# Optimization experiments

Measured on AMD Instinct MI355X. Metric: run time of the kernel, lower is better.

## Reference

```python
import jax, jax.numpy as jnp
import numpy as np

D_MODEL = 512
N_HEADS = 8
MAX_CH = 128
LN_EPS = 1e-5


def setup_inputs() -> dict:
    key = jax.random.key(0)
    ks = jax.random.split(key, 8)
    B, T, C, D = 8, 256, 64, D_MODEL
    x = jax.random.normal(ks[0], (B, T, C, D), dtype=jnp.float32)
    # nn.MultiheadAttention params: packed in_proj [3D, D], out_proj [D, D]
    in_proj_w = jax.random.normal(ks[1], (3 * D, D), dtype=jnp.float32) * 0.02
    in_proj_b = jnp.zeros((3 * D,), dtype=jnp.float32)
    out_proj_w = jax.random.normal(ks[2], (D, D), dtype=jnp.float32) * 0.02
    out_proj_b = jnp.zeros((D,), dtype=jnp.float32)
    ln_g = jnp.ones((D,), dtype=jnp.float32)
    ln_b = jnp.zeros((D,), dtype=jnp.float32)
    rel_pos_bias = jax.random.normal(ks[3], (N_HEADS, MAX_CH, MAX_CH), dtype=jnp.float32) * 0.02
    return {"x": x, "in_proj_w": in_proj_w, "in_proj_b": in_proj_b,
            "out_proj_w": out_proj_w, "out_proj_b": out_proj_b,
            "ln_g": ln_g, "ln_b": ln_b, "rel_pos_bias": rel_pos_bias}


def _layernorm(x, g, b):
    mu = jnp.mean(x, axis=-1, keepdims=True)
    var = jnp.var(x, axis=-1, keepdims=True)
    return (x - mu) * jax.lax.rsqrt(var + LN_EPS) * g + b


def reference(x, in_proj_w, in_proj_b, out_proj_w, out_proj_b, ln_g, ln_b, rel_pos_bias):
    B, T, C, D = x.shape
    H = N_HEADS
    hd = D // H
    N = B * T
    xf = x.reshape(N, C, D)
    # 2D additive attn_mask: mean over heads of rel-pos bias, broadcast over heads/batch
    bias = jnp.mean(rel_pos_bias[:, :C, :C], axis=0)  # [C, C]
    qkv = xf @ in_proj_w.T + in_proj_b  # [N, C, 3D]
    q, k, v = jnp.split(qkv, 3, axis=-1)
    q = q.reshape(N, C, H, hd)
    k = k.reshape(N, C, H, hd)
    v = v.reshape(N, C, H, hd)
    scores = jnp.einsum('nqhd,nkhd->nhqk', q, k) / jnp.sqrt(jnp.float32(hd))
    scores = scores + bias[None, None, :, :]
    attn = jax.nn.softmax(scores, axis=-1)
    ctx = jnp.einsum('nhqk,nkhd->nqhd', attn, v).reshape(N, C, D)
    attn_out = ctx @ out_proj_w.T + out_proj_b
    out = _layernorm(xf + attn_out, ln_g, ln_b)
    return out.reshape(B, T, C, D)
```

## Files before the change

kernel.cpp:

```cpp
#include <hip/hip_runtime.h>
#include <stdint.h>
#include <stddef.h>


typedef __attribute__((ext_vector_type(8))) short short8;
typedef __attribute__((ext_vector_type(4))) float f32x4;

typedef __attribute__((address_space(3))) unsigned int as3_u32;
typedef __attribute__((address_space(1))) unsigned int as1_u32;

#define VMCNT5  asm volatile("s_waitcnt vmcnt(5)" ::: "memory")
#define VMCNT2  asm volatile("s_waitcnt vmcnt(2)" ::: "memory")
#define VMCNT0  asm volatile("s_waitcnt vmcnt(0)" ::: "memory")
#define LGKM0   asm volatile("s_waitcnt lgkmcnt(0)" ::: "memory")
#define BARR()  __builtin_amdgcn_s_barrier()
#define PRIO1   __builtin_amdgcn_s_setprio(1)
#define PRIO0   __builtin_amdgcn_s_setprio(0)

__device__ __forceinline__ unsigned short f2bf(float f) {
  unsigned u = __builtin_bit_cast(unsigned, f);
  u = (u + 0x7FFFu + ((u >> 16) & 1u)) >> 16;
  return (unsigned short)u;
}

__device__ __forceinline__ f32x4 mfma16(short8 a, short8 b, f32x4 c) {
  return __builtin_amdgcn_mfma_f32_16x16x32_bf16(a, b, c, 0, 0, 0);
}

__device__ __forceinline__ short8 rd8s(const char* buf, int row, int unit) {
  return *(const short8*)(buf + row * 128 + ((unit ^ (row & 7)) * 16));
}
__device__ __forceinline__ void wr2s(char* buf, int row, int col, unsigned short v) {
  int slot = (col >> 3) ^ (row & 7);
  *(unsigned short*)(buf + row * 128 + slot * 16 + (col & 7) * 2) = v;
}
__device__ __forceinline__ void wr8s(char* buf, int row, int col, uint2 v) {
  int slot = (col >> 3) ^ (row & 7);
  *(uint2*)(buf + row * 128 + slot * 16 + (col & 7) * 2) = v;
}

__device__ __forceinline__ void stage8w(char* lds, const char* gsrc, int w, int lane) {
  __builtin_amdgcn_global_load_lds((const as1_u32*)(gsrc + w * 1024 + lane * 16),
                                   (as3_u32*)(lds + w * 1024), 16, 0, 0);
}

__device__ __forceinline__ void stage16k(char* ldsbase, const char* gsrc, int w, int lane) {
#pragma unroll
  for (int j = 0; j < 4; ++j) {
    int off = j * 4096 + w * 1024;
    __builtin_amdgcn_global_load_lds((const as1_u32*)(gsrc + off + lane * 16),
                                     (as3_u32*)(ldsbase + off), 16, 0, 0);
  }
}

__global__ void prep_kernel(const float* __restrict__ x,
                            const float* __restrict__ wqkv_f,
                            const float* __restrict__ wo_f,
                            const float* __restrict__ rel,
                            unsigned short* __restrict__ wt,
                            float* __restrict__ bias2d,
                            char* __restrict__ dout) {
  int b = blockIdx.x, tid = threadIdx.x;
  if (b < 8192) {
    int n = b >> 2, p = b & 3;
    char* dstb = dout + (size_t)n * 131072 + 65536;
    const float* srcb = x + (size_t)n * 32768;
#pragma unroll
    for (int t = 0; t < 4; ++t) {
      int flat = t * 256 + tid;
      int c = p * 2 + (flat >> 9);
      int r512 = flat & 511;
      int row = r512 >> 3, u = r512 & 7;
      const float* src = srcb + row * 512 + c * 64 + u * 8;
      float4 a = *(const float4*)src;
      float4 cc = *(const float4*)(src + 4);
      unsigned p0 = (unsigned)f2bf(a.x) | ((unsigned)f2bf(a.y) << 16);
      unsigned p1 = (unsigned)f2bf(a.z) | ((unsigned)f2bf(a.w) << 16);
      unsigned p2 = (unsigned)f2bf(cc.x) | ((unsigned)f2bf(cc.y) << 16);
      unsigned p3 = (unsigned)f2bf(cc.z) | ((unsigned)f2bf(cc.w) << 16);
      *(uint4*)(dstb + c * 8192 + u * 1024 + row * 16) = make_uint4(p0, p1, p2, p3);
    }
  } else if (b < 8288) {
    int cb2 = (b - 8192) * 2;
#pragma unroll
    for (int t = 0; t < 4; ++t) {
      int flat = t * 256 + tid;
      int c = cb2 + (flat >> 9);
      int r512 = flat & 511;
      int row = r512 >> 3, us = r512 & 7;
      int kg = us ^ (row & 7);
      int h = c / 24, j = c % 24;
      int kc = j / 3, rg = j % 3;
      const float* src =
          wqkv_f + (size_t)(rg * 512 + h * 64 + row) * 512 + kc * 64 + kg * 8;
      float4 a = *(const float4*)src;
      float4 cc = *(const float4*)(src + 4);
      unsigned p0 = (unsigned)f2bf(a.x) | ((unsigned)f2bf(a.y) << 16);
      unsigned p1 = (unsigned)f2bf(a.z) | ((unsigned)f2bf(a.w) << 16);
      unsigned p2 = (unsigned)f2bf(cc.x) | ((unsigned)f2bf(cc.y) << 16);
      unsigned p3 = (unsigned)f2bf(cc.z) | ((unsigned)f2bf(cc.w) << 16);
      *(uint4*)(wt + (size_t)c * 4096 + r512 * 8) = make_uint4(p0, p1, p2, p3);
    }
  } else if (b < 8320) {
    int cw = b - 8288;
    unsigned short* dst = wt + 786432 + (size_t)cw * 8192;
#pragma unroll
    for (int t = 0; t < 4; ++t) {
      int u = t * 256 + tid;
      int row = u >> 4, us = u & 15;
      int kg = (us & 8) | ((us ^ row) & 7);
      int kcw = cw >> 3, ng = cw & 7;
      const float* src = wo_f + (size_t)(ng * 64 + row) * 512 + kcw * 128 + kg * 8;
      float4 a = *(const float4*)src;
      float4 cc = *(const float4*)(src + 4);
      unsigned p0 = (unsigned)f2bf(a.x) | ((unsigned)f2bf(a.y) << 16);
      unsigned p1 = (unsigned)f2bf(a.z) | ((unsigned)f2bf(a.w) << 16);
      unsigned p2 = (unsigned)f2bf(cc.x) | ((unsigned)f2bf(cc.y) << 16);
      unsigned p3 = (unsigned)f2bf(cc.z) | ((unsigned)f2bf(cc.w) << 16);
      *(uint4*)(dst + u * 8) = make_uint4(p0, p1, p2, p3);
    }
  } else {
    int idx = (b - 8320) * 256 + tid;
    int m = idx >> 6, nn = idx & 63;
    float s = 0.f;
#pragma unroll
    for (int hh = 0; hh < 8; ++hh) s += rel[hh * 16384 + m * 128 + nn];
    bias2d[idx] = s * 0.125f;
  }
}

__global__ __launch_bounds__(512) void attn_qkv2(
    const char* __restrict__ wq,
    const float* __restrict__ bqkv,
    const float* __restrict__ bias2d,
    char* __restrict__ ctxg) {
  extern __shared__ __attribute__((aligned(16))) char smem[];
  char* RING = smem;
  char* XB   = smem + 32768;
  char* SCb  = smem + 49152;
  float* BQ  = (float*)(smem + 98304);

  const int tid = threadIdx.x;
  const int w = tid >> 6, lane = tid & 63;
  const int l15 = lane & 15, g = lane >> 4;
  const int ws = w >> 2;
  const int wn = w & 3;
  const int n0 = blockIdx.x * 2;

  const char* x0 = ctxg + (size_t)n0 * 131072 + 65536;
  const char* x1 = x0 + 131072;
  char* B0 = SCb + ws * 24576;
  char* B1 = B0 + 8192;
  char* B2 = B0 + 16384;

  const int brow = wn * 16 + l15;
  const int us0 = (g ^ (brow & 7)) * 16;
  const int us1 = ((4 + g) ^ (brow & 7)) * 16;
  const int mrow = wn * 16 + g * 4;
  const int wrow = wn * 16 + l15;

#pragma unroll
  for (int i = 0; i < 3; ++i) BQ[i * 512 + tid] = bqkv[i * 512 + tid];
  float b2d[16];
#pragma unroll
  for (int nt = 0; nt < 4; ++nt)
#pragma unroll
    for (int r = 0; r < 4; ++r)
      b2d[nt * 4 + r] = bias2d[(mrow + r) * 64 + nt * 16 + l15];
  VMCNT0; LGKM0; BARR();

  stage8w(XB, x0, w, lane);
  stage8w(XB + 8192, x1, w, lane);
  stage8w(RING, wq, w, lane);
  stage8w(RING + 8192, wq + 8192, w, lane);
  stage8w(RING + 16384, wq + 16384, w, lane);

  for (int h = 0; h < 8; ++h) {
    f32x4 aq[4] = {}, ak[4] = {}, av[4] = {};
#pragma unroll
    for (int kc = 0; kc < 8; ++kc) {
      const int j = h * 24 + kc * 3;
      const int sQ = (kc * 3) & 3, sK = (kc * 3 + 1) & 3, sV = (kc * 3 + 2) & 3;
      const int tQ = (kc * 3 + 3) & 3, tK = (kc * 3 + 4) & 3, tV = (kc * 3 + 5) & 3;
      { int c = j + 3; if (c > 191) c = 191;
        stage8w(RING + tQ * 8192, wq + (size_t)c * 8192, w, lane); }
      VMCNT2; BARR();
      short8 xa[8];
      { const char* xb = XB + ws * 8192;
#pragma unroll
        for (int mt = 0; mt < 4; ++mt)
#pragma unroll
          for (int ks = 0; ks < 2; ++ks)
            xa[mt * 2 + ks] = *(const short8*)(xb + (ks * 4 + g) * 1024 +
                                               (mt * 16 + l15) * 16);
      }
      {
        const char* wsl = RING + sQ * 8192;
        short8 bf0 = *(const short8*)(wsl + brow * 128 + us0);
        short8 bf1 = *(const short8*)(wsl + brow * 128 + us1);
        PRIO1;
#pragma unroll
        for (int mt = 0; mt < 4; ++mt) {
          aq[mt] = mfma16(xa[mt * 2], bf0, aq[mt]);
          aq[mt] = mfma16(xa[mt * 2 + 1], bf1, aq[mt]);
        }
        PRIO0;
      }
      { int c = j + 4; if (c > 191) c = 191;
        stage8w(RING + tK * 8192, wq + (size_t)c * 8192, w, lane); }
      BARR();
      {
        const char* wsl = RING + sK * 8192;
        short8 bf0 = *(const short8*)(wsl + brow * 128 + us0);
        short8 bf1 = *(const short8*)(wsl + brow * 128 + us1);
        PRIO1;
#pragma unroll
        for (int mt = 0; mt < 4; ++mt) {
          ak[mt] = mfma16(xa[mt * 2], bf0, ak[mt]);
          ak[mt] = mfma16(xa[mt * 2 + 1], bf1, ak[mt]);
        }
        PRIO0;
      }
      { int k2 = (kc + 1) & 7;
        stage8w(XB, x0 + (size_t)k2 * 8192, w, lane);
        stage8w(XB + 8192, x1 + (size_t)k2 * 8192, w, lane); }
      { int c = j + 5; if (c > 191) c = 191;
        stage8w(RING + tV * 8192, wq + (size_t)c * 8192, w, lane); }
      VMCNT5; BARR();
      {
        const char* wsl = RING + sV * 8192;
        short8 bf0 = *(const short8*)(wsl + brow * 128 + us0);
        short8 bf1 = *(const short8*)(wsl + brow * 128 + us1);
        PRIO1;
#pragma unroll
        for (int mt = 0; mt < 4; ++mt) {
          av[mt] = mfma16(xa[mt * 2], bf0, av[mt]);
          av[mt] = mfma16(xa[mt * 2 + 1], bf1, av[mt]);
        }
        PRIO0;
      }
    }

    {
      int col = wn * 16 + l15;
      float bq = BQ[h * 64 + col];
      float bk = BQ[512 + h * 64 + col];
      float bv = BQ[1024 + h * 64 + col];
#pragma unroll
      for (int mt = 0; mt < 4; ++mt) {
        int rowb = mt * 16 + g * 4;
#pragma unroll
        for (int r = 0; r < 4; ++r) {
          wr2s(B0, rowb + r, col, f2bf(aq[mt][r] + bq));
          wr2s(B1, rowb + r, col, f2bf(ak[mt][r] + bk));
        }
        unsigned short p0 = f2bf(av[mt][0] + bv);
        unsigned short p1 = f2bf(av[mt][1] + bv);
        unsigned short p2 = f2bf(av[mt][2] + bv);
        unsigned short p3 = f2bf(av[mt][3] + bv);
        unsigned lo = (unsigned)p0 | ((unsigned)p1 << 16);
        unsigned hi = (unsigned)p2 | ((unsigned)p3 << 16);
        wr8s(B2, col, rowb, make_uint2(lo, hi));
      }
    }
    LGKM0; BARR();

    {
      f32x4 sc[4] = {};
      short8 aq0 = rd8s(B0, wrow, g);
      short8 aq1 = rd8s(B0, wrow, 4 + g);
#pragma unroll
      for (int nt = 0; nt < 4; ++nt)
        sc[nt] = mfma16(aq0, rd8s(B1, nt * 16 + l15, g), sc[nt]);
#pragma unroll
      for (int nt = 0; nt < 4; ++nt)
        sc[nt] = mfma16(aq1, rd8s(B1, nt * 16 + l15, 4 + g), sc[nt]);
      float mx[4] = {-1e30f, -1e30f, -1e30f, -1e30f};
#pragma unroll
      for (int nt = 0; nt < 4; ++nt)
#pragma unroll
        for (int r = 0; r < 4; ++r) {
          float v = sc[nt][r] * 0.125f + b2d[nt * 4 + r];
          sc[nt][r] = v;
          mx[r] = fmaxf(mx[r], v);
        }
#pragma unroll
      for (int mk = 1; mk < 16; mk <<= 1)
#pragma unroll
        for (int r = 0; r < 4; ++r) mx[r] = fmaxf(mx[r], __shfl_xor(mx[r], mk));
      float sm[4] = {0.f, 0.f, 0.f, 0.f};
#pragma unroll
      for (int nt = 0; nt < 4; ++nt)
#pragma unroll
        for (int r = 0; r < 4; ++r) {
          float e = __expf(sc[nt][r] - mx[r]);
          sc[nt][r] = e;
          sm[r] += e;
        }
#pragma unroll
      for (int mk = 1; mk < 16; mk <<= 1)
#pragma unroll
        for (int r = 0; r < 4; ++r) sm[r] += __shfl_xor(sm[r], mk);
      float inv[4];
#pragma unroll
      for (int r = 0; r < 4; ++r) inv[r] = 1.0f / sm[r];
#pragma unroll
      for (int nt = 0; nt < 4; ++nt)
#pragma unroll
        for (int r = 0; r < 4; ++r)
          wr2s(B0, mrow + r, nt * 16 + l15, f2bf(sc[nt][r] * inv[r]));
    }

    f32x4 cv[4] = {};
    {
      short8 ap0 = rd8s(B0, wrow, g);
      short8 ap1 = rd8s(B0, wrow, 4 + g);
#pragma unroll
      for (int nt = 0; nt < 4; ++nt)
        cv[nt] = mfma16(ap0, rd8s(B2, nt * 16 + l15, g), cv[nt]);
#pragma unroll
      for (int nt = 0; nt < 4; ++nt)
        cv[nt] = mfma16(ap1, rd8s(B2, nt * 16 + l15, 4 + g), cv[nt]);
    }
    BARR();
#pragma unroll
    for (int nt = 0; nt < 4; ++nt)
#pragma unroll
      for (int r = 0; r < 4; ++r)
        wr2s(B1, mrow + r, nt * 16 + l15, f2bf(cv[nt][r]));
    LGKM0; BARR();

    {
      char* cdst = ctxg + (size_t)(n0 + ws) * 131072 + h * 8192;
      int gt = tid & 255;
#pragma unroll
      for (int it = 0; it < 2; ++it) {
        int flat = it * 256 + gt;
        int row = flat >> 3, s = flat & 7;
        uint4 v = *(const uint4*)(B1 + row * 128 + s * 16);
        *(uint4*)(cdst + row * 128 + s * 16) = v;
      }
    }
  }
}

__global__ __launch_bounds__(256, 2) void oproj_ln(
    const char* __restrict__ ctxg,
    const char* __restrict__ wo,
    const float* __restrict__ bo,
    const float* __restrict__ x,
    const float* __restrict__ lng,
    const float* __restrict__ lnb,
    float* __restrict__ out) {
  __shared__ __attribute__((aligned(16))) char smem[65536];
  char* WB = smem;
  char* CB = smem + 32768;
  float* EP  = (float*)smem;
  float* SM1 = (float*)(smem + 32768);
  float* SM2 = (float*)(smem + 33408);

  const int n = blockIdx.x;
  const int tid = threadIdx.x;
  const int w = tid >> 6, lane = tid & 63;
  const int l15 = lane & 15, g = lane >> 4;
  const int um = w >> 1, un = w & 1;

  const char* cbase = ctxg + (size_t)n * 131072;

  stage16k(CB, cbase, w, lane);
  stage16k(WB, wo, w, lane);

  f32x4 acc[8][2][2] = {};

  for (int kc = 0; kc < 4; ++kc) {
    short8 actx[2][4];
#pragma unroll
    for (int ng = 0; ng < 8; ++ng) {
      int b = kc * 8 + ng;
      if (b < 31)
        stage16k(WB + (((b + 1) & 1) << 14), wo + (size_t)(b + 1) * 16384, w, lane);
      if ((ng & 1) == 0 && kc < 3) {
        int p = ng >> 1;
        int off = p * 4096 + w * 1024;
        __builtin_amdgcn_global_load_lds(
            (const as1_u32*)(cbase + (kc + 1) * 16384 + off + lane * 16),
            (as3_u32*)(CB + (((kc + 1) & 1) << 14) + off), 16, 0, 0);
      }
      if (b < 31) { VMCNT5; } else { VMCNT0; }
      BARR();
      const char* cb = CB + ((kc & 1) << 14);
      if (ng == 0) {
#pragma unroll
        for (int mt = 0; mt < 2; ++mt)
#pragma unroll
          for (int ks = 0; ks < 4; ++ks) {
            int row = um * 32 + mt * 16 + l15;
            int u = ks * 4 + g;
            actx[mt][ks] = *(const short8*)(cb + (u >> 3) * 8192 + row * 128 +
                                            (((u & 7) ^ (row & 7)) * 16));
          }
      }
      const char* wsl = WB + ((b & 1) << 14);
      PRIO1;
#pragma unroll
      for (int ks = 0; ks < 4; ++ks) {
#pragma unroll
        for (int nt = 0; nt < 2; ++nt) {
          int row = un * 32 + nt * 16 + l15;
          int kg = ks * 4 + g;
          int us = (kg & 8) | ((kg ^ row) & 7);
          short8 bfr = *(const short8*)(wsl + row * 256 + us * 16);
          acc[ng][0][nt] = mfma16(actx[0][ks], bfr, acc[ng][0][nt]);
          acc[ng][1][nt] = mfma16(actx[1][ks], bfr, acc[ng][1][nt]);
        }
      }
      PRIO0;
      BARR();
    }
  }

  VMCNT0;
  const float* xblk = x + (size_t)n * 32768;
  float* oblk = out + (size_t)n * 32768;
  float s1[2][4] = {}, s2[2][4] = {};

#pragma unroll
  for (int ng = 0; ng < 8; ++ng) {
#pragma unroll
    for (int t = 0; t < 4; ++t) {
      int flat = t * 256 + tid;
      int row = flat >> 4, f4 = flat & 15;
      float4 v = *(const float4*)(xblk + row * 512 + ng * 64 + f4 * 4);
      *(float4*)(EP + row * 68 + f4 * 4) = v;
    }
    LGKM0; BARR();
    float boA[2];
#pragma unroll
    for (int nt = 0; nt < 2; ++nt) boA[nt] = bo[ng * 64 + un * 32 + nt * 16 + l15];
#pragma unroll
    for (int mt = 0; mt < 2; ++mt)
#pragma unroll
      for (int nt = 0; nt < 2; ++nt)
#pragma unroll
        for (int r = 0; r < 4; ++r) {
          int row = um * 32 + mt * 16 + g * 4 + r;
          float xv = EP[row * 68 + un * 32 + nt * 16 + l15];
          float v = acc[ng][mt][nt][r] + boA[nt] + xv;
          acc[ng][mt][nt][r] = v;
          s1[mt][r] += v;
          s2[mt][r] += v * v;
        }
    LGKM0; BARR();
  }
#pragma unroll
  for (int mk = 1; mk < 16; mk <<= 1)
#pragma unroll
    for (int mt = 0; mt < 2; ++mt)
#pragma unroll
      for (int r = 0; r < 4; ++r) {
        s1[mt][r] += __shfl_xor(s1[mt][r], mk);
        s2[mt][r] += __shfl_xor(s2[mt][r], mk);
      }
  if (l15 == 0) {
#pragma unroll
    for (int mt = 0; mt < 2; ++mt)
#pragma unroll
      for (int r = 0; r < 4; ++r) {
        int row = um * 32 + mt * 16 + g * 4 + r;
        SM1[row * 2 + un] = s1[mt][r];
        SM2[row * 2 + un] = s2[mt][r];
      }
  }
  LGKM0; BARR();
  float mu[2][4], rs[2][4];
#pragma unroll
  for (int mt = 0; mt < 2; ++mt)
#pragma unroll
    for (int r = 0; r < 4; ++r) {
      int row = um * 32 + mt * 16 + g * 4 + r;
      float a1 = SM1[row * 2] + SM1[row * 2 + 1];
      float a2 = SM2[row * 2] + SM2[row * 2 + 1];
      float m = a1 * (1.0f / 512.0f);
      float var = a2 * (1.0f / 512.0f) - m * m;
      mu[mt][r] = m;
      rs[mt][r] = rsqrtf(var + 1e-5f);
    }
  BARR();
#pragma unroll
  for (int ng = 0; ng < 8; ++ng) {
    float lgA[2], lbA[2];
#pragma unroll
    for (int nt = 0; nt < 2; ++nt) {
      int col = ng * 64 + un * 32 + nt * 16 + l15;
      lgA[nt] = lng[col];
      lbA[nt] = lnb[col];
    }
#pragma unroll
    for (int mt = 0; mt < 2; ++mt)
#pragma unroll
      for (int nt = 0; nt < 2; ++nt)
#pragma unroll
        for (int r = 0; r < 4; ++r) {
          int row = um * 32 + mt * 16 + g * 4 + r;
          EP[row * 68 + un * 32 + nt * 16 + l15] =
              (acc[ng][mt][nt][r] - mu[mt][r]) * rs[mt][r] * lgA[nt] + lbA[nt];
        }
    LGKM0; BARR();
#pragma unroll
    for (int t = 0; t < 4; ++t) {
      int flat = t * 256 + tid;
      int row = flat >> 4, f4 = flat & 15;
      *(float4*)(oblk + row * 512 + ng * 64 + f4 * 4) =
          *(const float4*)(EP + row * 68 + f4 * 4);
    }
    BARR();
  }
}

extern "C" void kernel_launch(void* const* d_in, const int* in_sizes, int n_in,
                              void* d_out, int out_size, void* d_ws, size_t ws_size,
                              hipStream_t stream) {
  const float* x    = (const float*)d_in[0];
  const float* wqkv = (const float*)d_in[1];
  const float* bqkv = (const float*)d_in[2];
  const float* wo   = (const float*)d_in[3];
  const float* bo   = (const float*)d_in[4];
  const float* lng  = (const float*)d_in[5];
  const float* lnb  = (const float*)d_in[6];
  const float* rel  = (const float*)d_in[7];

  unsigned short* wt = (unsigned short*)d_ws;
  float* bias2d = (float*)((char*)d_ws + 2097152);
  const char* wqc = (const char*)d_ws;
  const char* woc = (const char*)d_ws + 1572864;

  hipFuncSetAttribute(reinterpret_cast<const void*>(attn_qkv2),
                      hipFuncAttributeMaxDynamicSharedMemorySize, 104448);

  prep_kernel<<<8336, 256, 0, stream>>>(x, wqkv, wo, rel, wt, bias2d,
                                        (char*)d_out);
  attn_qkv2<<<1024, 512, 104448, stream>>>(wqc, bqkv, bias2d, (char*)d_out);
  oproj_ln<<<2048, 256, 0, stream>>>((const char*)d_out, woc, bo, x, lng, lnb,
                                     (float*)d_out);
}
```

Measured before the change: 550.7 us.

## Double-buffer QKV weight slabs, load X directly to registers, shrink LDS

The QKV projection loop now stages all three Q/K/V weight slices per k-chunk into a two-slot ring. It drops the LDS staging of X and prefetches the next X fragments straight from global into a second register set. The attention scratch buffers now alias the weight ring, cutting static LDS from about 104KB to 55KB so more blocks could fit per CU. The aim is fewer barriers per chunk and better overlap of loads with MFMA. The cost is higher register pressure from the double register set, and the bias is reloaded every head.

After: 890.4 us. 1.62x slower.

```diff
diff --git a/kernel.cpp b/kernel.cpp
--- a/kernel.cpp
+++ b/kernel.cpp
@@ -9,8 +9,8 @@
 typedef __attribute__((address_space(3))) unsigned int as3_u32;
 typedef __attribute__((address_space(1))) unsigned int as1_u32;
 
+#define VMCNT11 asm volatile("s_waitcnt vmcnt(11)" ::: "memory")
 #define VMCNT5  asm volatile("s_waitcnt vmcnt(5)" ::: "memory")
-#define VMCNT2  asm volatile("s_waitcnt vmcnt(2)" ::: "memory")
 #define VMCNT0  asm volatile("s_waitcnt vmcnt(0)" ::: "memory")
 #define LGKM0   asm volatile("s_waitcnt lgkmcnt(0)" ::: "memory")
 #define BARR()  __builtin_amdgcn_s_barrier()
@@ -43,6 +43,11 @@
   __builtin_amdgcn_global_load_lds((const as1_u32*)(gsrc + w * 1024 + lane * 16),
                                    (as3_u32*)(lds + w * 1024), 16, 0, 0);
 }
+__device__ __forceinline__ void stage24(char* lds, const char* gsrc, int w, int lane) {
+  stage8w(lds, gsrc, w, lane);
+  stage8w(lds + 8192, gsrc + 8192, w, lane);
+  stage8w(lds + 16384, gsrc + 16384, w, lane);
+}
 
 __device__ __forceinline__ void stage16k(char* ldsbase, const char* gsrc, int w, int lane) {
 #pragma unroll
@@ -51,6 +56,47 @@
     __builtin_amdgcn_global_load_lds((const as1_u32*)(gsrc + off + lane * 16),
                                      (as3_u32*)(ldsbase + off), 16, 0, 0);
   }
+}
+
+__device__ __forceinline__ void load_xa(short8* xa, const char* xb, int l15, int g) {
+#pragma unroll
+  for (int mt = 0; mt < 4; ++mt)
+#pragma unroll
+    for (int ks = 0; ks < 2; ++ks)
+      xa[mt * 2 + ks] = *(const short8*)(xb + (ks * 4 + g) * 1024 +
+                                         (mt * 16 + l15) * 16);
+}
+
+__device__ __forceinline__ void kc_body(int h, int kc, const char* wq,
+                                        const char* xb, char* RING,
+                                        int w, int lane, int brow,
+                                        int us0, int us1, int l15, int g,
+                                        short8* cur, short8* nxt,
+                                        f32x4* aq, f32x4* ak, f32x4* av) {
+  if (kc < 7) {
+    stage24(RING + ((kc + 1) & 1) * 24576,
+            wq + (size_t)(h * 24 + (kc + 1) * 3) * 8192, w, lane);
+    load_xa(nxt, xb + (size_t)(kc + 1) * 8192, l15, g);
+    VMCNT11;
+  } else {
+    VMCNT0;
+  }
+  BARR();
+  const char* slot = RING + (kc & 1) * 24576;
+  PRIO1;
+#pragma unroll
+  for (int rg = 0; rg < 3; ++rg) {
+    const char* wsl = slot + rg * 8192;
+    short8 bf0 = *(const short8*)(wsl + brow * 128 + us0);
+    short8 bf1 = *(const short8*)(wsl + brow * 128 + us1);
+    f32x4* acc = (rg == 0) ? aq : (rg == 1) ? ak : av;
+#pragma unroll
+    for (int mt = 0; mt < 4; ++mt) {
+      acc[mt] = mfma16(cur[mt * 2], bf0, acc[mt]);
+      acc[mt] = mfma16(cur[mt * 2 + 1], bf1, acc[mt]);
+    }
+  }
+  PRIO0;
 }
 
 __global__ void prep_kernel(const float* __restrict__ x,
@@ -134,11 +180,9 @@
     const float* __restrict__ bqkv,
     const float* __restrict__ bias2d,
     char* __restrict__ ctxg) {
-  extern __shared__ __attribute__((aligned(16))) char smem[];
+  __shared__ __attribute__((aligned(16))) char smem[55296];
   char* RING = smem;
-  char* XB   = smem + 32768;
-  char* SCb  = smem + 49152;
-  float* BQ  = (float*)(smem + 98304);
+  float* BQ  = (float*)(smem + 49152);
 
   const int tid = threadIdx.x;
   const int w = tid >> 6, lane = tid & 63;
@@ -147,9 +191,8 @@
   const int wn = w & 3;
   const int n0 = blockIdx.x * 2;
 
-  const char* x0 = ctxg + (size_t)n0 * 131072 + 65536;
-  const char* x1 = x0 + 131072;
-  char* B0 = SCb + ws * 24576;
+  const char* xb = ctxg + (size_t)(n0 + ws) * 131072 + 65536;
+  char* B0 = smem + ws * 24576;
   char* B1 = B0 + 8192;
   char* B2 = B0 + 16384;
 
@@ -161,85 +204,29 @@
 
 #pragma unroll
   for (int i = 0; i < 3; ++i) BQ[i * 512 + tid] = bqkv[i * 512 + tid];
-  float b2d[16];
-#pragma unroll
-  for (int nt = 0; nt < 4; ++nt)
-#pragma unroll
-    for (int r = 0; r < 4; ++r)
-      b2d[nt * 4 + r] = bias2d[(mrow + r) * 64 + nt * 16 + l15];
   VMCNT0; LGKM0; BARR();
 
-  stage8w(XB, x0, w, lane);
-  stage8w(XB + 8192, x1, w, lane);
-  stage8w(RING, wq, w, lane);
-  stage8w(RING + 8192, wq + 8192, w, lane);
-  stage8w(RING + 16384, wq + 16384, w, lane);
+  short8 xaA[8], xaB[8];
+  stage24(RING, wq, w, lane);
+  load_xa(xaA, xb, l15, g);
 
   for (int h = 0; h < 8; ++h) {
     f32x4 aq[4] = {}, ak[4] = {}, av[4] = {};
 #pragma unroll
-    for (int kc = 0; kc < 8; ++kc) {
-      const int j = h * 24 + kc * 3;
-      const int sQ = (kc * 3) & 3, sK = (kc * 3 + 1) & 3, sV = (kc * 3 + 2) & 3;
-      const int tQ = (kc * 3 + 3) & 3, tK = (kc * 3 + 4) & 3, tV = (kc * 3 + 5) & 3;
-      { int c = j + 3; if (c > 191) c = 191;
-        stage8w(RING + tQ * 8192, wq + (size_t)c * 8192, w, lane); }
-      VMCNT2; BARR();
-      short8 xa[8];
-      { const char* xb = XB + ws * 8192;
-#pragma unroll
-        for (int mt = 0; mt < 4; ++mt)
-#pragma unroll
-          for (int ks = 0; ks < 2; ++ks)
-            xa[mt * 2 + ks] = *(const short8*)(xb + (ks * 4 + g) * 1024 +
-                                               (mt * 16 + l15) * 16);
-      }
-      {
-        const char* wsl = RING + sQ * 8192;
-        short8 bf0 = *(const short8*)(wsl + brow * 128 + us0);
-        short8 bf1 = *(const short8*)(wsl + brow * 128 + us1);
-        PRIO1;
-#pragma unroll
-        for (int mt = 0; mt < 4; ++mt) {
-          aq[mt] = mfma16(xa[mt * 2], bf0, aq[mt]);
-          aq[mt] = mfma16(xa[mt * 2 + 1], bf1, aq[mt]);
-        }
-        PRIO0;
-      }
-      { int c = j + 4; if (c > 191) c = 191;
-        stage8w(RING + tK * 8192, wq + (size_t)c * 8192, w, lane); }
-      BARR();
-      {
-        const char* wsl = RING + sK * 8192;
-        short8 bf0 = *(const short8*)(wsl + brow * 128 + us0);
-        short8 bf1 = *(const short8*)(wsl + brow * 128 + us1);
-        PRIO1;
-#pragma unroll
-        for (int mt = 0; mt < 4; ++mt) {
-          ak[mt] = mfma16(xa[mt * 2], bf0, ak[mt]);
-          ak[mt] = mfma16(xa[mt * 2 + 1], bf1, ak[mt]);
-        }
-        PRIO0;
-      }
-      { int k2 = (kc + 1) & 7;
-        stage8w(XB, x0 + (size_t)k2 * 8192, w, lane);
-        stage8w(XB + 8192, x1 + (size_t)k2 * 8192, w, lane); }
-      { int c = j + 5; if (c > 191) c = 191;
-        stage8w(RING + tV * 8192, wq + (size_t)c * 8192, w, lane); }
-      VMCNT5; BARR();
-      {
-        const char* wsl = RING + sV * 8192;
-        short8 bf0 = *(const short8*)(wsl + brow * 128 + us0);
-        short8 bf1 = *(const short8*)(wsl + brow * 128 + us1);
-        PRIO1;
-#pragma unroll
-        for (int mt = 0; mt < 4; ++mt) {
-          av[mt] = mfma16(xa[mt * 2], bf0, av[mt]);
-          av[mt] = mfma16(xa[mt * 2 + 1], bf1, av[mt]);
-        }
-        PRIO0;
-      }
-    }
+    for (int kp = 0; kp < 4; ++kp) {
+      kc_body(h, kp * 2, wq, xb, RING, w, lane, brow, us0, us1, l15, g,
+              xaA, xaB, aq, ak, av);
+      kc_body(h, kp * 2 + 1, wq, xb, RING, w, lane, brow, us0, us1, l15, g,
+              xaB, xaA, aq, ak, av);
+    }
+    BARR();
+
+    float b2dv[16];
+#pragma unroll
+    for (int nt = 0; nt < 4; ++nt)
+#pragma unroll
+      for (int r = 0; r < 4; ++r)
+        b2dv[nt * 4 + r] = bias2d[(mrow + r) * 64 + nt * 16 + l15];
 
     {
       int col = wn * 16 + l15;
@@ -280,7 +267,7 @@
       for (int nt = 0; nt < 4; ++nt)
 #pragma unroll
         for (int r = 0; r < 4; ++r) {
-          float v = sc[nt][r] * 0.125f + b2d[nt * 4 + r];
+          float v = sc[nt][r] * 0.125f + b2dv[nt * 4 + r];
           sc[nt][r] = v;
           mx[r] = fmaxf(mx[r], v);
         }
@@ -340,6 +327,11 @@
         uint4 v = *(const uint4*)(B1 + row * 128 + s * 16);
         *(uint4*)(cdst + row * 128 + s * 16) = v;
       }
+    }
+    BARR();
+    if (h < 7) {
+      stage24(RING, wq + (size_t)((h + 1) * 24) * 8192, w, lane);
+      load_xa(xaA, xb, l15, g);
     }
   }
 }
@@ -534,12 +526,9 @@
   const char* wqc = (const char*)d_ws;
   const char* woc = (const char*)d_ws + 1572864;
 
-  hipFuncSetAttribute(reinterpret_cast<const void*>(attn_qkv2),
-                      hipFuncAttributeMaxDynamicSharedMemorySize, 104448);
-
   prep_kernel<<<8336, 256, 0, stream>>>(x, wqkv, wo, rel, wt, bias2d,
                                         (char*)d_out);
-  attn_qkv2<<<1024, 512, 104448, stream>>>(wqc, bqkv, bias2d, (char*)d_out);
+  attn_qkv2<<<1024, 512, 0, stream>>>(wqc, bqkv, bias2d, (char*)d_out);
   oproj_ln<<<2048, 256, 0, stream>>>((const char*)d_out, woc, bo, x, lng, lnb,
                                      (float*)d_out);
 }
```

## Alias attention scratch onto staging ring to halve LDS and raise occupancy

Applied to the files above, without the earlier changes.

The fused QKV+attention kernel's LDS footprint shrinks from about 102KB dynamic to 54KB static. The per-head Q/K/V/score scratch now overlays the weight ring and X staging buffers instead of occupying a separate region. To make this safe, the last k-chunk stops prefetching, fully drains outstanding loads, and adds barriers. The next head's initial ring and X tiles are then staged only after the attention/output phase finishes. This should let two 512-thread blocks fit per CU, but it loses the cross-head prefetch overlap and adds synchronization.

Result: no change. 556.8 us (+1.1%).

```diff
diff --git a/kernel.cpp b/kernel.cpp
--- a/kernel.cpp
+++ b/kernel.cpp
@@ -11,6 +11,7 @@
 
 #define VMCNT5  asm volatile("s_waitcnt vmcnt(5)" ::: "memory")
 #define VMCNT2  asm volatile("s_waitcnt vmcnt(2)" ::: "memory")
+#define VMCNT1  asm volatile("s_waitcnt vmcnt(1)" ::: "memory")
 #define VMCNT0  asm volatile("s_waitcnt vmcnt(0)" ::: "memory")
 #define LGKM0   asm volatile("s_waitcnt lgkmcnt(0)" ::: "memory")
 #define BARR()  __builtin_amdgcn_s_barrier()
@@ -134,11 +135,10 @@
     const float* __restrict__ bqkv,
     const float* __restrict__ bias2d,
     char* __restrict__ ctxg) {
-  extern __shared__ __attribute__((aligned(16))) char smem[];
+  __shared__ __attribute__((aligned(16))) char smem[55296];
   char* RING = smem;
   char* XB   = smem + 32768;
-  char* SCb  = smem + 49152;
-  float* BQ  = (float*)(smem + 98304);
+  float* BQ  = (float*)(smem + 49152);
 
   const int tid = threadIdx.x;
   const int w = tid >> 6, lane = tid & 63;
@@ -149,7 +149,7 @@
 
   const char* x0 = ctxg + (size_t)n0 * 131072 + 65536;
   const char* x1 = x0 + 131072;
-  char* B0 = SCb + ws * 24576;
+  char* B0 = smem + ws * 24576;
   char* B1 = B0 + 8192;
   char* B2 = B0 + 16384;
 
@@ -182,9 +182,13 @@
       const int j = h * 24 + kc * 3;
       const int sQ = (kc * 3) & 3, sK = (kc * 3 + 1) & 3, sV = (kc * 3 + 2) & 3;
       const int tQ = (kc * 3 + 3) & 3, tK = (kc * 3 + 4) & 3, tV = (kc * 3 + 5) & 3;
-      { int c = j + 3; if (c > 191) c = 191;
-        stage8w(RING + tQ * 8192, wq + (size_t)c * 8192, w, lane); }
-      VMCNT2; BARR();
+      if (kc < 7) {
+        stage8w(RING + tQ * 8192, wq + (size_t)(j + 3) * 8192, w, lane);
+        VMCNT2;
+      } else {
+        VMCNT1;
+      }
+      BARR();
       short8 xa[8];
       { const char* xb = XB + ws * 8192;
 #pragma unroll
@@ -206,8 +210,8 @@
         }
         PRIO0;
       }
-      { int c = j + 4; if (c > 191) c = 191;
-        stage8w(RING + tK * 8192, wq + (size_t)c * 8192, w, lane); }
+      if (kc < 7)
+        stage8w(RING + tK * 8192, wq + (size_t)(j + 4) * 8192, w, lane);
       BARR();
       {
         const char* wsl = RING + sK * 8192;
@@ -221,12 +225,17 @@
         }
         PRIO0;
       }
-      { int k2 = (kc + 1) & 7;
-        stage8w(XB, x0 + (size_t)k2 * 8192, w, lane);
-        stage8w(XB + 8192, x1 + (size_t)k2 * 8192, w, lane); }
-      { int c = j + 5; if (c > 191) c = 191;
-        stage8w(RING + tV * 8192, wq + (size_t)c * 8192, w, lane); }
-      VMCNT5; BARR();
+      if (kc < 7) {
+        stage8w(XB, x0 + (size_t)(kc + 1) * 8192, w, lane);
+        stage8w(XB + 8192, x1 + (size_t)(kc + 1) * 8192, w, lane);
+      }
+      if (kc < 7) {
+        stage8w(RING + tV * 8192, wq + (size_t)(j + 5) * 8192, w, lane);
+        VMCNT5;
+      } else {
+        VMCNT0;
+      }
+      BARR();
       {
         const char* wsl = RING + sV * 8192;
         short8 bf0 = *(const short8*)(wsl + brow * 128 + us0);
@@ -240,6 +249,7 @@
         PRIO0;
       }
     }
+    BARR();
 
     {
       int col = wn * 16 + l15;
@@ -340,6 +350,15 @@
         uint4 v = *(const uint4*)(B1 + row * 128 + s * 16);
         *(uint4*)(cdst + row * 128 + s * 16) = v;
       }
+    }
+    BARR();
+    if (h < 7) {
+      const char* wn_ = wq + (size_t)((h + 1) * 24) * 8192;
+      stage8w(XB, x0, w, lane);
+      stage8w(XB + 8192, x1, w, lane);
+      stage8w(RING, wn_, w, lane);
+      stage8w(RING + 8192, wn_ + 8192, w, lane);
+      stage8w(RING + 16384, wn_ + 16384, w, lane);
     }
   }
 }
@@ -534,12 +553,9 @@
   const char* wqc = (const char*)d_ws;
   const char* woc = (const char*)d_ws + 1572864;
 
-  hipFuncSetAttribute(reinterpret_cast<const void*>(attn_qkv2),
-                      hipFuncAttributeMaxDynamicSharedMemorySize, 104448);
-
   prep_kernel<<<8336, 256, 0, stream>>>(x, wqkv, wo, rel, wt, bias2d,
                                         (char*)d_out);
-  attn_qkv2<<<1024, 512, 104448, stream>>>(wqc, bqkv, bias2d, (char*)d_out);
+  attn_qkv2<<<1024, 512, 0, stream>>>(wqc, bqkv, bias2d, (char*)d_out);
   oproj_ln<<<2048, 256, 0, stream>>>((const char*)d_out, woc, bo, x, lng, lnb,
                                      (float*)d_out);
 }
```
